# Kernel tuning notes

Measured on AMD Instinct MI355X. Metric: run time of the kernel, lower is better.

## Reference

```python
import jax, jax.numpy as jnp
import numpy as np

D_MODEL = 2048
N_HEAD = 16
SEM_DIM = 1024
GEO_DIM = 1024
ATTN_DIM = 2048
ROPE_BASE = 10000.0


def _rope(x, base=ROPE_BASE):
    # x: [B, H, S, d] with even d; GPT-NeoX rotate-half convention
    S, d = x.shape[-2], x.shape[-1]
    inv_freq = 1.0 / (base ** (jnp.arange(0, d, 2, dtype=jnp.float32) / d))
    t = jnp.arange(S, dtype=jnp.float32)
    freqs = jnp.einsum('s,f->sf', t, inv_freq)  # [S, d/2]
    cos, sin = jnp.cos(freqs), jnp.sin(freqs)
    x1, x2 = x[..., : d // 2], x[..., d // 2 :]
    return jnp.concatenate([x1 * cos - x2 * sin, x1 * sin + x2 * cos], axis=-1).astype(x.dtype)


def _split_heads(y, H):
    B, S, dim = y.shape
    return y.reshape(B, S, H, dim // H).transpose(0, 2, 1, 3)  # [B,H,S,hd]


def setup_inputs() -> dict:
    key = jax.random.key(0)
    ks = jax.random.split(key, 7)
    B, S = 2, 2048
    sd = 0.02
    return {
        'x': jax.random.normal(ks[0], (B, S, D_MODEL), dtype=jnp.float32),
        'Wq_sem': jax.random.normal(ks[1], (SEM_DIM, D_MODEL), dtype=jnp.float32) * sd,
        'Wk_sem': jax.random.normal(ks[2], (SEM_DIM, D_MODEL), dtype=jnp.float32) * sd,
        'Wq_geo': jax.random.normal(ks[3], (GEO_DIM, D_MODEL), dtype=jnp.float32) * sd,
        'Wk_geo': jax.random.normal(ks[4], (GEO_DIM, D_MODEL), dtype=jnp.float32) * sd,
        'Wv': jax.random.normal(ks[5], (ATTN_DIM, D_MODEL), dtype=jnp.float32) * sd,
        'Wo': jax.random.normal(ks[6], (D_MODEL, ATTN_DIM), dtype=jnp.float32) * sd,
    }


def reference(x, Wq_sem, Wk_sem, Wq_geo, Wk_geo, Wv, Wo):
    B, S, _ = x.shape
    H = N_HEAD
    # decoupled projections (nn.Linear: y = x @ W.T)
    q_sem = _split_heads(x @ Wq_sem.T, H)  # [B,H,S,64]
    k_sem = _split_heads(x @ Wk_sem.T, H)
    q_geo = _rope(_split_heads(x @ Wq_geo.T, H))  # RoPE only on geo part
    k_geo = _rope(_split_heads(x @ Wk_geo.T, H))
    v = _split_heads(x @ Wv.T, H)  # [B,H,S,128]
    # concatenated decoupled q/k -> single fused score (fp32), SDPA default scale
    q = jnp.concatenate([q_sem, q_geo], axis=-1)
    k = jnp.concatenate([k_sem, k_geo], axis=-1)
    scale = 1.0 / jnp.sqrt(jnp.asarray(q.shape[-1], dtype=jnp.float32))
    scores = jnp.einsum('bhqd,bhkd->bhqk', q, k).astype(jnp.float32) * scale
    causal = jnp.tril(jnp.ones((S, S), dtype=bool))
    scores = jnp.where(causal, scores, jnp.finfo(jnp.float32).min)
    attn = jax.nn.softmax(scores, axis=-1).astype(v.dtype)
    out = jnp.einsum('bhqk,bhkd->bhqd', attn, v)  # [B,H,S,128]
    out = out.transpose(0, 2, 1, 3).reshape(B, S, ATTN_DIM)
    return out @ Wo.T  # [B,S,d_model]
```

## Files before the change

kernel.cpp:

```cpp
#include <hip/hip_runtime.h>
#include <cstdint>
#include <cstddef>

typedef unsigned short u16;
typedef __attribute__((ext_vector_type(8))) short bf16x8;
typedef __attribute__((ext_vector_type(4))) float f32x4;

#define MFMA32(a, b, c) __builtin_amdgcn_mfma_f32_16x16x32_bf16(a, b, c, 0, 0, 0)

__device__ __forceinline__ u16 f2b(float f) {
  union { float f; unsigned u; } v; v.f = f;
  unsigned u = v.u;
  return (u16)((u + 0x7fffu + ((u >> 16) & 1u)) >> 16);
}
__device__ __forceinline__ float b2f(u16 h) {
  union { unsigned u; float f; } v; v.u = ((unsigned)h) << 16;
  return v.f;
}

__device__ __forceinline__ void g2l16(const void* g, void* l) {
  __builtin_amdgcn_global_load_lds((__attribute__((address_space(1))) void*)(g),
                                   (__attribute__((address_space(3))) void*)(l), 16, 0, 0);
}

__global__ __launch_bounds__(256) void cast_f2b_v4(const float* __restrict__ in,
                                                   u16* __restrict__ out, int n4) {
  int i = blockIdx.x * 256 + threadIdx.x;
  if (i >= n4) return;
  float4 v = ((const float4*)in)[i];
  ushort4 r;
  r.x = f2b(v.x); r.y = f2b(v.y); r.z = f2b(v.z); r.w = f2b(v.w);
  ((ushort4*)out)[i] = r;
}

template <bool BF16_OUT>
__global__ __launch_bounds__(256) void gemm_bt(const u16* __restrict__ A,
                                               const u16* __restrict__ B,
                                               void* __restrict__ C, int N, int K) {
  __shared__ u16 As[128 * 64];
  __shared__ u16 Bs[128 * 64];
  const int tid = threadIdx.x;
  const int wid = tid >> 6;
  const int lane = tid & 63;
  const int lm = lane & 15;
  const int quad = lane >> 4;
  const int r3 = lm & 7;
  const int wm = (wid & 1) * 64;
  const int wn = (wid >> 1) * 64;
  const int bm = blockIdx.y * 128;
  const int bn = blockIdx.x * 128;

  const u16* Ab = A + (size_t)bm * K;
  const u16* Bb = B + (size_t)bn * K;

  f32x4 zero = {0.f, 0.f, 0.f, 0.f};
  f32x4 acc[4][4];
#pragma unroll
  for (int i = 0; i < 4; ++i)
#pragma unroll
    for (int j = 0; j < 4; ++j) acc[i][j] = zero;

  for (int k0 = 0; k0 < K; k0 += 64) {
#pragma unroll
    for (int it = 0; it < 4; ++it) {
      int c = it * 256 + tid;
      int rg = c >> 6, rw = (c >> 3) & 7, u = c & 7;
      int row = rg * 8 + rw;
      int chd = u ^ rw;
      g2l16(Ab + (size_t)row * K + k0 + chd * 8, As + c * 8);
      g2l16(Bb + (size_t)row * K + k0 + chd * 8, Bs + c * 8);
    }
    __syncthreads();
#pragma unroll
    for (int ks = 0; ks < 2; ++ks) {
      bf16x8 a[4], b[4];
      int chd = ks * 4 + quad;
#pragma unroll
      for (int i = 0; i < 4; ++i) {
        int row = wm + i * 16 + lm;
        a[i] = *(const bf16x8*)(As + (((row >> 3) * 64 + r3 * 8 + (chd ^ r3)) * 8));
      }
#pragma unroll
      for (int j = 0; j < 4; ++j) {
        int row = wn + j * 16 + lm;
        b[j] = *(const bf16x8*)(Bs + (((row >> 3) * 64 + r3 * 8 + (chd ^ r3)) * 8));
      }
#pragma unroll
      for (int i = 0; i < 4; ++i)
#pragma unroll
        for (int j = 0; j < 4; ++j)
          acc[i][j] = MFMA32(a[i], b[j], acc[i][j]);
    }
    __syncthreads();
  }

#pragma unroll
  for (int i = 0; i < 4; ++i)
#pragma unroll
    for (int j = 0; j < 4; ++j)
#pragma unroll
      for (int r = 0; r < 4; ++r) {
        int row = bm + wm + i * 16 + quad * 4 + r;
        int col = bn + wn + j * 16 + lm;
        float v = acc[i][j][r];
        if (BF16_OUT)
          ((u16*)C)[(size_t)row * N + col] = f2b(v);
        else
          ((float*)C)[(size_t)row * N + col] = v;
      }
}

__global__ __launch_bounds__(256) void rope_rearrange_v2(const u16* __restrict__ Y,
                                                         u16* __restrict__ Q,
                                                         u16* __restrict__ Kb,
                                                         u16* __restrict__ VT) {
  const float SC = 0.12751744f;
  __shared__ u16 T[128][68];
  const int st = blockIdx.x;
  const int bh = blockIdx.y;
  const int b = bh >> 4, h = bh & 15;
  const int tid = threadIdx.x;
  const int d = tid & 127;
  const int sgrp = tid >> 7;

  float inv = 0.f;
  const int f0 = d & 31;
  if (d >= 64) inv = __powf(10000.0f, -(float)(2 * f0) * (1.0f / 64.0f));

  const u16* Yc = Y + (size_t)(b * 2048 + st * 64) * 6144;

#pragma unroll 4
  for (int k = 0; k < 32; ++k) {
    const int sl = sgrp * 32 + k;
    const int s = st * 64 + sl;
    const u16* Yr = Yc + (size_t)sl * 6144;

    T[d][sl] = Yr[4096 + h * 128 + d];

    float qv, kv;
    if (d < 64) {
      qv = b2f(Yr[h * 64 + d]);
      kv = b2f(Yr[1024 + h * 64 + d]);
    } else {
      float ang = (float)s * inv;
      float sn = sinf(ang), cs = cosf(ang);
      float qx1 = b2f(Yr[2048 + h * 64 + f0]);
      float qx2 = b2f(Yr[2048 + h * 64 + f0 + 32]);
      float kx1 = b2f(Yr[3072 + h * 64 + f0]);
      float kx2 = b2f(Yr[3072 + h * 64 + f0 + 32]);
      if (d < 96) { qv = qx1 * cs - qx2 * sn; kv = kx1 * cs - kx2 * sn; }
      else        { qv = qx1 * sn + qx2 * cs; kv = kx1 * sn + kx2 * cs; }
    }
    size_t qo = ((size_t)bh * 2048 + s) * 128 + d;
    Q[qo] = f2b(qv * SC);
    Kb[qo] = f2b(kv);
  }
  __syncthreads();

#pragma unroll
  for (int it = 0; it < 8; ++it) {
    const int i = it * 256 + tid;
    const int dd = i >> 4;
    const int ch = i & 15;
    ushort4 v = *(const ushort4*)(&T[dd][ch * 4]);
    *(ushort4*)(VT + ((size_t)bh * 128 + dd) * 2048 + st * 64 + ch * 4) = v;
  }
}

__global__ __launch_bounds__(256, 3) void attn_v4(const u16* __restrict__ Q,
                                                  const u16* __restrict__ K,
                                                  const u16* __restrict__ VT,
                                                  u16* __restrict__ O) {
  constexpr int S = 2048;
  constexpr int D = 128;
  __shared__ u16 Ks[64 * 128];
  __shared__ u16 Vs[128 * 64];
  __shared__ u16 Ps[64 * 72];
  const int bx = blockIdx.x;
  const int bh = blockIdx.y;
  const int b = bh >> 4, h = bh & 15;
  const int tid = threadIdx.x, wid = tid >> 6, lane = tid & 63;
  const int lm = lane & 15, quad = lane >> 4;
  const int rx = lm & 7;
  const int wrow = wid * 16;

#pragma unroll 1
  for (int pass = 0; pass < 2; ++pass) {
    const int qt = pass == 0 ? bx : 31 - bx;

    bf16x8 aq[4];
#pragma unroll
    for (int ks = 0; ks < 4; ++ks)
      aq[ks] = *(const bf16x8*)(Q + ((size_t)bh * S + (size_t)qt * 64 + wrow + lm) * D +
                                ks * 32 + quad * 8);

    float l_r[4] = {0.f, 0.f, 0.f, 0.f};
    f32x4 zero = {0.f, 0.f, 0.f, 0.f};
    f32x4 oacc[8];
#pragma unroll
    for (int t = 0; t < 8; ++t) oacc[t] = zero;

    for (int kt = 0; kt <= qt; ++kt) {
      __syncthreads();
      const u16* Kt = K + ((size_t)bh * S + (size_t)kt * 64) * D;
#pragma unroll
      for (int it = 0; it < 4; ++it) {
        int c = it * 256 + tid;
        int row = c >> 4, u = c & 15;
        g2l16(Kt + (size_t)row * 128 + (size_t)(u ^ (row & 7)) * 8, Ks + c * 8);
      }
      const u16* Vt = VT + (size_t)bh * D * S + (size_t)kt * 64;
#pragma unroll
      for (int it = 0; it < 4; ++it) {
        int c = it * 256 + tid;
        int row = c >> 3, u = c & 7;
        g2l16(Vt + (size_t)row * S + (size_t)(u ^ (row & 7)) * 8, Vs + c * 8);
      }
      __syncthreads();

      f32x4 sc[4];
#pragma unroll
      for (int j = 0; j < 4; ++j) sc[j] = zero;
      __builtin_amdgcn_s_setprio(1);
#pragma unroll
      for (int ks = 0; ks < 4; ++ks) {
        const int kc = ks * 4 + quad;
#pragma unroll
        for (int j = 0; j < 4; ++j) {
          bf16x8 bk = *(const bf16x8*)(Ks + (((j * 16 + lm) * 16 + (kc ^ rx)) * 8));
          sc[j] = MFMA32(aq[ks], bk, sc[j]);
        }
      }
      __builtin_amdgcn_s_setprio(0);

      const bool diag = (kt == qt);
#pragma unroll
      for (int r = 0; r < 4; ++r) {
        const int qcol = wrow + quad * 4 + r;
        float pv[4];
        float rs = 0.f;
#pragma unroll
        for (int j = 0; j < 4; ++j) {
          float p = __builtin_amdgcn_exp2f(fminf(sc[j][r], 30.0f));
          if (diag && (j * 16 + lm > qcol)) p = 0.f;
          rs += p;
          pv[j] = p;
        }
#pragma unroll
        for (int dd = 1; dd < 16; dd <<= 1) rs += __shfl_xor(rs, dd);
        l_r[r] += rs;
        const int prow = (wrow + quad * 4 + r) * 72;
#pragma unroll
        for (int j = 0; j < 4; ++j) Ps[prow + j * 16 + lm] = f2b(pv[j]);
      }
      __syncthreads();

      __builtin_amdgcn_s_setprio(1);
#pragma unroll
      for (int ks = 0; ks < 2; ++ks) {
        bf16x8 ap = *(const bf16x8*)(Ps + (wrow + lm) * 72 + ks * 32 + quad * 8);
        const int kc = ks * 4 + quad;
#pragma unroll
        for (int t = 0; t < 8; ++t) {
          bf16x8 bv = *(const bf16x8*)(Vs + (((t * 16 + lm) * 8 + (kc ^ rx)) * 8));
          oacc[t] = MFMA32(ap, bv, oacc[t]);
        }
      }
      __builtin_amdgcn_s_setprio(0);
    }

#pragma unroll
    for (int r = 0; r < 4; ++r) {
      float inv = 1.0f / l_r[r];
      const int srow = qt * 64 + wrow + quad * 4 + r;
      u16* Orow = O + ((size_t)b * S + srow) * 2048 + h * 128;
#pragma unroll
      for (int t = 0; t < 8; ++t) Orow[t * 16 + lm] = f2b(oacc[t][r] * inv);
    }
  }
}

extern "C" void kernel_launch(void* const* d_in, const int* in_sizes, int n_in,
                              void* d_out, int out_size, void* d_ws, size_t ws_size,
                              hipStream_t stream) {
  const float* x      = (const float*)d_in[0];
  const float* Wq_sem = (const float*)d_in[1];
  const float* Wk_sem = (const float*)d_in[2];
  const float* Wq_geo = (const float*)d_in[3];
  const float* Wk_geo = (const float*)d_in[4];
  const float* Wv     = (const float*)d_in[5];
  const float* Wo     = (const float*)d_in[6];

  char* ws = (char*)d_ws;
  u16* xb   = (u16*)(ws);
  u16* Wall = (u16*)(ws + 16777216);
  u16* Wob  = (u16*)(ws + 16777216 + 25165824);
  u16* Y    = (u16*)(ws + 16777216 + 25165824 + 8388608);
  u16* Qb   = xb;
  u16* Ob   = Wall;
  u16* Kb   = (u16*)d_out;
  u16* VT   = (u16*)((char*)d_out + 16777216);

  cast_f2b_v4<<<8192, 256, 0, stream>>>(x, xb, 2097152);
  cast_f2b_v4<<<2048, 256, 0, stream>>>(Wq_sem, Wall + 0 * 2097152, 524288);
  cast_f2b_v4<<<2048, 256, 0, stream>>>(Wk_sem, Wall + 1 * 2097152, 524288);
  cast_f2b_v4<<<2048, 256, 0, stream>>>(Wq_geo, Wall + 2 * 2097152, 524288);
  cast_f2b_v4<<<2048, 256, 0, stream>>>(Wk_geo, Wall + 3 * 2097152, 524288);
  cast_f2b_v4<<<4096, 256, 0, stream>>>(Wv,     Wall + 4 * 2097152, 1048576);
  cast_f2b_v4<<<4096, 256, 0, stream>>>(Wo, Wob, 1048576);

  gemm_bt<true><<<dim3(48, 32), 256, 0, stream>>>(xb, Wall, Y, 6144, 2048);

  rope_rearrange_v2<<<dim3(32, 32), 256, 0, stream>>>(Y, Qb, Kb, VT);

  attn_v4<<<dim3(16, 32), 256, 0, stream>>>(Qb, Kb, VT, Ob);

  gemm_bt<false><<<dim3(16, 32), 256, 0, stream>>>(Ob, Wob, d_out, 2048, 2048);
}
```

Baseline: 412.0 us.

## Read K and V tiles directly from global memory in attention, dropping LDS staging

The attention kernel no longer stages K and V tiles into shared memory with async global-to-LDS copies. Each wave now loads its MFMA B-operands straight from global memory, which removes the two block-wide barriers per key tile and the P-tile barrier, and relaxes launch bounds to 2 blocks per CU. The aim is to cut synchronisation and LDS traffic. In exchange, every wave re-reads the full K and V tiles (four times the global/L2 traffic), and the V^T reads are strided by the sequence length, so coalescing is poor and the kernel leans heavily on cache hit rates.

```diff
diff --git a/kernel.cpp b/kernel.cpp
--- a/kernel.cpp
+++ b/kernel.cpp
@@ -167,22 +167,22 @@
   }
 }
 
-__global__ __launch_bounds__(256, 3) void attn_v4(const u16* __restrict__ Q,
+__global__ __launch_bounds__(256, 2) void attn_v6(const u16* __restrict__ Q,
                                                   const u16* __restrict__ K,
                                                   const u16* __restrict__ VT,
                                                   u16* __restrict__ O) {
   constexpr int S = 2048;
   constexpr int D = 128;
-  __shared__ u16 Ks[64 * 128];
-  __shared__ u16 Vs[128 * 64];
   __shared__ u16 Ps[64 * 72];
   const int bx = blockIdx.x;
   const int bh = blockIdx.y;
   const int b = bh >> 4, h = bh & 15;
   const int tid = threadIdx.x, wid = tid >> 6, lane = tid & 63;
   const int lm = lane & 15, quad = lane >> 4;
-  const int rx = lm & 7;
   const int wrow = wid * 16;
+
+  const u16* Kbh = K + (size_t)bh * S * D;
+  const u16* Vbh = VT + (size_t)bh * D * S;
 
 #pragma unroll 1
   for (int pass = 0; pass < 2; ++pass) {
@@ -200,23 +200,10 @@
 #pragma unroll
     for (int t = 0; t < 8; ++t) oacc[t] = zero;
 
+#pragma unroll 1
     for (int kt = 0; kt <= qt; ++kt) {
-      __syncthreads();
-      const u16* Kt = K + ((size_t)bh * S + (size_t)kt * 64) * D;
-#pragma unroll
-      for (int it = 0; it < 4; ++it) {
-        int c = it * 256 + tid;
-        int row = c >> 4, u = c & 15;
-        g2l16(Kt + (size_t)row * 128 + (size_t)(u ^ (row & 7)) * 8, Ks + c * 8);
-      }
-      const u16* Vt = VT + (size_t)bh * D * S + (size_t)kt * 64;
-#pragma unroll
-      for (int it = 0; it < 4; ++it) {
-        int c = it * 256 + tid;
-        int row = c >> 3, u = c & 7;
-        g2l16(Vt + (size_t)row * S + (size_t)(u ^ (row & 7)) * 8, Vs + c * 8);
-      }
-      __syncthreads();
+      const u16* Kt = Kbh + (size_t)kt * 64 * D;
+      const u16* Vt = Vbh + (size_t)kt * 64;
 
       f32x4 sc[4];
 #pragma unroll
@@ -224,10 +211,9 @@
       __builtin_amdgcn_s_setprio(1);
 #pragma unroll
       for (int ks = 0; ks < 4; ++ks) {
-        const int kc = ks * 4 + quad;
 #pragma unroll
         for (int j = 0; j < 4; ++j) {
-          bf16x8 bk = *(const bf16x8*)(Ks + (((j * 16 + lm) * 16 + (kc ^ rx)) * 8));
+          bf16x8 bk = *(const bf16x8*)(Kt + (j * 16 + lm) * D + ks * 32 + quad * 8);
           sc[j] = MFMA32(aq[ks], bk, sc[j]);
         }
       }
@@ -253,16 +239,14 @@
 #pragma unroll
         for (int j = 0; j < 4; ++j) Ps[prow + j * 16 + lm] = f2b(pv[j]);
       }
-      __syncthreads();
 
       __builtin_amdgcn_s_setprio(1);
 #pragma unroll
       for (int ks = 0; ks < 2; ++ks) {
         bf16x8 ap = *(const bf16x8*)(Ps + (wrow + lm) * 72 + ks * 32 + quad * 8);
-        const int kc = ks * 4 + quad;
 #pragma unroll
         for (int t = 0; t < 8; ++t) {
-          bf16x8 bv = *(const bf16x8*)(Vs + (((t * 16 + lm) * 8 + (kc ^ rx)) * 8));
+          bf16x8 bv = *(const bf16x8*)(Vt + (size_t)(t * 16 + lm) * S + ks * 32 + quad * 8);
           oacc[t] = MFMA32(ap, bv, oacc[t]);
         }
       }
@@ -313,7 +297,7 @@
 
   rope_rearrange_v2<<<dim3(32, 32), 256, 0, stream>>>(Y, Qb, Kb, VT);
 
-  attn_v4<<<dim3(16, 32), 256, 0, stream>>>(Qb, Kb, VT, Ob);
+  attn_v6<<<dim3(16, 32), 256, 0, stream>>>(Qb, Kb, VT, Ob);
 
   gemm_bt<false><<<dim3(16, 32), 256, 0, stream>>>(Ob, Wob, d_out, 2048, 2048);
 }
```

Result: slower. 609.5 us (+48.0%).
